# Kernel optimization log

Hardware: AMD Instinct MI355X
Metric: run time of the kernel (lower is better)

The kernel has to match this reference:

```python
import jax, jax.numpy as jnp
import numpy as np

B, H, S, D = 4, 16, 1024, 64


def setup_inputs() -> dict:
    key = jax.random.key(0)
    kq, kk, kv, kw = jax.random.split(key, 4)
    xq = jax.random.normal(kq, (B, H, S, D), dtype=jnp.float32)
    xk = jax.random.normal(kk, (B, H, S, D), dtype=jnp.float32)
    xv = jax.random.normal(kv, (B, H, S, D), dtype=jnp.float32)
    # wpsm: nn.Linear(n_heads, n_heads, bias=False) weight, shape [H_out, H_in]
    bound = 1.0 / np.sqrt(H)
    W = jax.random.uniform(kw, (H, H), minval=-bound, maxval=bound, dtype=jnp.float32)
    return {"xq": xq, "xk": xk, "xv": xv, "W": W, "causal": 1}


def reference(xq, xk, xv, W, causal):
    head_dim = xq.shape[-1]
    sq, sk = xq.shape[-2], xk.shape[-2]
    # QK^T scaled: [B, H, Sq, Sk]
    scores = jnp.einsum("bhqd,bhkd->bhqk", xq, xk) * jax.lax.rsqrt(jnp.float32(head_dim))
    # head-mixing linear over head axis: mixed[b,g,q,k] = sum_h W[g,h] * scores[b,h,q,k]
    scores = jnp.einsum("gh,bhqk->bgqk", W, scores)
    if causal:
        mask = jnp.triu(jnp.full((sq, sk), -jnp.inf, dtype=scores.dtype), k=1)
        scores = scores + mask  # broadcast over [B, H]
    probs = jax.nn.softmax(scores.astype(jnp.float32), axis=-1).astype(xq.dtype)
    out = jnp.einsum("bhqk,bhkd->bhqd", probs, xv)
    return out.transpose(0, 2, 1, 3)  # [B, Sq, H, D]
```

## Files before the change

### kernel.cpp

```cpp
#include <hip/hip_runtime.h>
#include <math.h>

#define NB 4
#define HH 16
#define SS 1024
#define DD 64
#define NKST 16

typedef __attribute__((ext_vector_type(8))) short bf16x8;
typedef __attribute__((ext_vector_type(4))) float f32x4;

static __device__ __forceinline__ short f2bf(float f) {
    __bf16 h = (__bf16)f;
    return __builtin_bit_cast(short, h);
}
static __device__ __forceinline__ float bflo(int w) {
    return __builtin_bit_cast(float, (unsigned)w << 16);
}
static __device__ __forceinline__ float bfhi(int w) {
    return __builtin_bit_cast(float, (unsigned)w & 0xffff0000u);
}
static __device__ __forceinline__ float bfu(unsigned short u) {
    return __builtin_bit_cast(float, (unsigned)u << 16);
}
static __device__ __forceinline__ int pidx(int pos, int hp) {
    int s = ((pos >> 2) & 3) | (((pos >> 9) & 1) << 2);
    return pos * 8 + (hp ^ s);
}
static __device__ __forceinline__ int midx(int g, int loc, int x3) {
    return g * 512 + ((((loc >> 2) ^ x3) << 2) | (loc & 3));
}

static __device__ __forceinline__ bf16x8 load8_bf16(const float* p) {
    const float4* p4 = reinterpret_cast<const float4*>(p);
    float4 a = p4[0], b = p4[1];
    bf16x8 f;
    f[0]=f2bf(a.x); f[1]=f2bf(a.y); f[2]=f2bf(a.z); f[3]=f2bf(a.w);
    f[4]=f2bf(b.x); f[5]=f2bf(b.y); f[6]=f2bf(b.z); f[7]=f2bf(b.w);
    return f;
}

__global__ __launch_bounds__(256) void prep_all(const float* __restrict__ xk,
                                                short* __restrict__ kfr,
                                                const float* __restrict__ xv,
                                                short* __restrict__ vfr) {
    __shared__ float T[64][65];
    const int bid = blockIdx.x;
    const int t = threadIdx.x;
    if (bid < 2048) {
        int c = bid * 256 + t;
        int lane = c & 63, ds = (c >> 6) & 1, kt = (c >> 7) & 3;
        int kst = (c >> 9) & 15, h = (c >> 13) & 15, b = c >> 17;
        const float* src = xk + ((size_t)((b * HH + h) * SS) + kst * 64 + kt * 16 + (lane & 15)) * DD
                              + ds * 32 + (lane >> 4) * 8;
        *(reinterpret_cast<bf16x8*>(kfr) + c) = load8_bf16(src);
    } else {
        int tile = bid - 2048;
        const float* src = xv + ((size_t)(tile >> 4) * SS + (tile & 15) * 64) * DD;
        int row = t >> 2, col = (t & 3) * 16;
#pragma unroll
        for (int ii = 0; ii < 4; ++ii) {
            float4 v = *reinterpret_cast<const float4*>(src + row * DD + col + ii * 4);
            T[row][col + ii*4] = v.x; T[row][col + ii*4 + 1] = v.y;
            T[row][col + ii*4 + 2] = v.z; T[row][col + ii*4 + 3] = v.w;
        }
        __syncthreads();
#pragma unroll
        for (int jj = 0; jj < 2; ++jj) {
            int c2 = t * 2 + jj;
            int lane = c2 & 63, nt = (c2 >> 6) & 3, kc = (c2 >> 8) & 1;
            bf16x8 o;
#pragma unroll
            for (int i = 0; i < 8; ++i)
                o[i] = f2bf(T[kc * 32 + (lane >> 4) * 8 + i][nt * 16 + (lane & 15)]);
            *(reinterpret_cast<bf16x8*>(vfr) + (size_t)tile * 512 + c2) = o;
        }
    }
}

__global__ __launch_bounds__(1024) void hca_fused(
    const float* __restrict__ xq, const short* __restrict__ kfr,
    const short* __restrict__ vfr, const float* __restrict__ Wm,
    const int* __restrict__ causalp, unsigned short* __restrict__ ppO,
    float2* __restrict__ ppml)
{
    __shared__ int Pbuf[8192];
    __shared__ int Mbuf[8192];

    const int tid  = threadIdx.x;
    const int lane = tid & 63;
    const int w    = tid >> 6;
    const int l15  = lane & 15;
    const int lg   = lane >> 4;

    const int bid  = blockIdx.x;
    const int b    = bid & 3;
    const int u    = (bid >> 2) & 63;
    const int r    = (bid >> 8) & 1;
    const int qt   = r ? u : 63 - u;
    const int kpar = u & 1;
    const int q0   = qt << 4;
    const int pairIdx = b * 64 + qt;

    const int causal = causalp[0];
    const int hp = w & 7;
    const int kh = w >> 3;
    const int g  = w;

    const float LOG2E = 1.44269504088896f;

    bf16x8 wt = {0,0,0,0,0,0,0,0};
    if (lg < 2) {
#pragma unroll
        for (int ii = 0; ii < 8; ++ii)
            wt[ii] = f2bf(Wm[l15 * 16 + lg * 8 + ii] * 0.125f * LOG2E);
    }

    const short* vb0 = vfr + (size_t)(b * HH + g) * NKST * 8 * 512 + lane * 8;
    const short* kb0 = kfr + (size_t)(b * HH + 2 * hp) * NKST * 8 * 512 + lane * 8;

    bf16x8 qf[2][2];
#pragma unroll
    for (int hi = 0; hi < 2; ++hi) {
        const float* qp = xq + ((size_t)(b * HH + 2 * hp + hi) * SS + q0 + l15) * DD + lg * 8;
#pragma unroll
        for (int ds = 0; ds < 2; ++ds) qf[hi][ds] = load8_bf16(qp + ds * 32);
    }

    f32x4 oacc[4];
#pragma unroll
    for (int nt = 0; nt < 4; ++nt) oacc[nt] = (f32x4){0.f, 0.f, 0.f, 0.f};
    float mrun = -INFINITY, lrun = 0.f;

    const int nkf = causal ? ((q0 + 16 + 63) >> 6) : NKST;

#pragma unroll 1
    for (int kst = kpar; kst < nkf; kst += 2) {
        const int k0 = kst << 6;

        const short* kbase = kb0 + (size_t)kst * 8 * 512;
        __builtin_amdgcn_s_setprio(1);
#pragma unroll
        for (int kt2 = 0; kt2 < 2; ++kt2) {
            const int kt = kh * 2 + kt2;
            f32x4 a0 = (f32x4){0.f,0.f,0.f,0.f}, a1 = a0;
#pragma unroll
            for (int ds = 0; ds < 2; ++ds) {
                bf16x8 kfa = *reinterpret_cast<const bf16x8*>(kbase + (kt*2 + ds) * 512);
                bf16x8 kfb = *reinterpret_cast<const bf16x8*>(kbase + (NKST*8 + kt*2 + ds) * 512);
                a0 = __builtin_amdgcn_mfma_f32_16x16x32_bf16(qf[0][ds], kfa, a0, 0, 0, 0);
                a1 = __builtin_amdgcn_mfma_f32_16x16x32_bf16(qf[1][ds], kfb, a1, 0, 0, 0);
            }
#pragma unroll
            for (int rr = 0; rr < 4; ++rr) {
                int pos = (lg * 4 + rr) * 64 + kt * 16 + l15;
                int pk = (int)(unsigned short)f2bf(a0[rr]) | ((int)(unsigned short)f2bf(a1[rr]) << 16);
                Pbuf[pidx(pos, hp)] = pk;
            }
        }
        __builtin_amdgcn_s_setprio(0);

        const short* vbase = vb0 + (size_t)kst * 8 * 512;
        bf16x8 vf[8];
#pragma unroll
        for (int kc = 0; kc < 2; ++kc)
#pragma unroll
            for (int nt = 0; nt < 4; ++nt)
                vf[kc * 4 + nt] = *reinterpret_cast<const bf16x8*>(vbase + (kc*4 + nt) * 512);

        __syncthreads();

#pragma unroll
        for (int m = 0; m < 4; ++m) {
            const int c = w * 4 + m;
            const int pos = c * 16 + l15;
            int4 ia = {0, 0, 0, 0};
            if (lg < 2) {
                ia.x = Pbuf[pidx(pos, lg * 4 + 0)];
                ia.y = Pbuf[pidx(pos, lg * 4 + 1)];
                ia.z = Pbuf[pidx(pos, lg * 4 + 2)];
                ia.w = Pbuf[pidx(pos, lg * 4 + 3)];
            }
            bf16x8 A = __builtin_bit_cast(bf16x8, ia);
            f32x4 cc = (f32x4){0.f, 0.f, 0.f, 0.f};
            cc = __builtin_amdgcn_mfma_f32_16x16x32_bf16(A, wt, cc, 0, 0, 0);
            int loc = w * 32 + (c & 3) * 8 + lg * 2;
            int x3 = (w + l15) & 7;
            int u0 = (int)(unsigned short)f2bf(cc[0]) | ((int)(unsigned short)f2bf(cc[1]) << 16);
            int u1 = (int)(unsigned short)f2bf(cc[2]) | ((int)(unsigned short)f2bf(cc[3]) << 16);
            *reinterpret_cast<int2*>(&Mbuf[midx(l15, loc, x3)]) = make_int2(u0, u1);
        }
        __syncthreads();

        const int x3r = (l15 + g) & 7;
        int4 rA = *reinterpret_cast<const int4*>(&Mbuf[midx(g, l15 * 32 + lg * 4, x3r)]);
        int4 rB = *reinterpret_cast<const int4*>(&Mbuf[midx(g, l15 * 32 + 16 + lg * 4, x3r)]);

        float sm[16];
#pragma unroll
        for (int jj = 0; jj < 4; ++jj) {
            sm[2*jj]     = bflo(rA[jj]);  sm[2*jj + 1] = bfhi(rA[jj]);
            sm[8 + 2*jj] = bflo(rB[jj]);  sm[9 + 2*jj] = bfhi(rB[jj]);
        }
        if (causal && kst == nkf - 1) {
#pragma unroll
            for (int jj = 0; jj < 16; ++jj) {
                int kk = (jj < 8) ? (lg * 8 + jj) : (32 + lg * 8 + (jj - 8));
                if (k0 + kk > q0 + l15) sm[jj] = -INFINITY;
            }
        }

        float mx[4];
#pragma unroll
        for (int t = 0; t < 4; ++t)
            mx[t] = fmaxf(fmaxf(sm[4*t], sm[4*t+1]), fmaxf(sm[4*t+2], sm[4*t+3]));
        float mt = fmaxf(fmaxf(mx[0], mx[1]), fmaxf(mx[2], mx[3]));
        mt = fmaxf(mt, __shfl_xor(mt, 16));
        mt = fmaxf(mt, __shfl_xor(mt, 32));

        if (__any(mt > mrun + 8.0f)) {
            float mnew = fmaxf(mrun, mt);
            float scl = __builtin_amdgcn_exp2f(mrun - mnew);
            mrun = mnew;
            lrun *= scl;
            int scli = __builtin_bit_cast(int, scl);
#pragma unroll
            for (int rr = 0; rr < 4; ++rr) {
                int v = __builtin_amdgcn_ds_bpermute((lg * 4 + rr) * 4, scli);
                float s = __builtin_bit_cast(float, v);
#pragma unroll
                for (int nt = 0; nt < 4; ++nt) oacc[nt][rr] *= s;
            }
        }

#pragma unroll
        for (int jj = 0; jj < 16; ++jj) sm[jj] = __builtin_amdgcn_exp2f(sm[jj] - mrun);
        float s0 = ((sm[0]+sm[1]) + (sm[2]+sm[3])) + ((sm[4]+sm[5]) + (sm[6]+sm[7]));
        float s1 = ((sm[8]+sm[9]) + (sm[10]+sm[11])) + ((sm[12]+sm[13]) + (sm[14]+sm[15]));
        lrun += s0 + s1;

        int paw[8];
#pragma unroll
        for (int t = 0; t < 8; ++t)
            paw[t] = (int)(unsigned short)f2bf(sm[2*t]) | ((int)(unsigned short)f2bf(sm[2*t+1]) << 16);
        bf16x8 pa0 = __builtin_bit_cast(bf16x8, *(int4*)&paw[0]);
        bf16x8 pa1 = __builtin_bit_cast(bf16x8, *(int4*)&paw[4]);

        __builtin_amdgcn_s_setprio(1);
#pragma unroll
        for (int nt = 0; nt < 4; ++nt)
            oacc[nt] = __builtin_amdgcn_mfma_f32_16x16x32_bf16(pa0, vf[nt], oacc[nt], 0, 0, 0);
#pragma unroll
        for (int nt = 0; nt < 4; ++nt)
            oacc[nt] = __builtin_amdgcn_mfma_f32_16x16x32_bf16(pa1, vf[4 + nt], oacc[nt], 0, 0, 0);
        __builtin_amdgcn_s_setprio(0);
    }

    float lt = lrun;
    lt += __shfl_xor(lt, 16);
    lt += __shfl_xor(lt, 32);
    if (lg == 0)
        ppml[(((size_t)pairIdx * 2 + kpar) * 16 + g) * 16 + l15] = make_float2(mrun, lt);
    float rl = (lt > 0.f) ? (1.0f / lt) : 0.f;
    int rli = __builtin_bit_cast(int, rl);
    size_t obase = (((size_t)pairIdx * 2 + kpar) * 16 + g) * 1024;
#pragma unroll
    for (int rr = 0; rr < 4; ++rr) {
        int v = __builtin_amdgcn_ds_bpermute((lg * 4 + rr) * 4, rli);
        float linv = __builtin_bit_cast(float, v);
        int q = lg * 4 + rr;
#pragma unroll
        for (int nt = 0; nt < 4; ++nt)
            ppO[obase + q * 64 + nt * 16 + l15] =
                (unsigned short)f2bf(oacc[nt][rr] * linv);
    }
}

__global__ __launch_bounds__(256) void hca_combine(
    const unsigned short* __restrict__ ppO, const float2* __restrict__ ppml,
    float* __restrict__ out)
{
    const int pairIdx = blockIdx.x;
    const int b = pairIdx >> 6, qt = pairIdx & 63;
    const int t = threadIdx.x;
    const int g = t >> 4, dc = t & 15;

    const size_t o0 = (((size_t)pairIdx * 2 + 0) * 16 + g) * 1024;
    const size_t o1 = (((size_t)pairIdx * 2 + 1) * 16 + g) * 1024;
    const float2* ml0p = ppml + (((size_t)pairIdx * 2 + 0) * 16 + g) * 16;
    const float2* ml1p = ppml + (((size_t)pairIdx * 2 + 1) * 16 + g) * 16;

#pragma unroll 4
    for (int q = 0; q < 16; ++q) {
        float2 ml0 = ml0p[q], ml1 = ml1p[q];
        float ms = fmaxf(ml0.x, ml1.x);
        float w0 = ml0.y * exp2f(ml0.x - ms);
        float w1 = ml1.y * exp2f(ml1.x - ms);
        float rs = 1.0f / (w0 + w1);
        float a0 = w0 * rs, a1 = w1 * rs;
        ushort4 u0 = *reinterpret_cast<const ushort4*>(ppO + o0 + q * 64 + dc * 4);
        ushort4 u1 = *reinterpret_cast<const ushort4*>(ppO + o1 + q * 64 + dc * 4);
        float4 res;
        res.x = a0 * bfu(u0.x) + a1 * bfu(u1.x);
        res.y = a0 * bfu(u0.y) + a1 * bfu(u1.y);
        res.z = a0 * bfu(u0.z) + a1 * bfu(u1.z);
        res.w = a0 * bfu(u0.w) + a1 * bfu(u1.w);
        *reinterpret_cast<float4*>(out + (((size_t)b * SS + qt * 16 + q) * HH + g) * DD + dc * 4) = res;
    }
}

extern "C" void kernel_launch(void* const* d_in, const int* in_sizes, int n_in,
                              void* d_out, int out_size, void* d_ws, size_t ws_size,
                              hipStream_t stream) {
    const float* xq = (const float*)d_in[0];
    const float* xk = (const float*)d_in[1];
    const float* xv = (const float*)d_in[2];
    const float* Wm = (const float*)d_in[3];
    const int* causal = (const int*)d_in[4];
    float* out = (float*)d_out;

    short* vfr = (short*)d_ws;
    short* kfr = vfr + (size_t)NB * HH * SS * DD;
    unsigned short* ppO = (unsigned short*)(kfr + (size_t)NB * HH * SS * DD);
    float2* ppml = (float2*)(ppO + (size_t)512 * 16 * 1024);

    prep_all<<<2048 + NB * HH * NKST, 256, 0, stream>>>(xk, kfr, xv, vfr);

    hca_fused<<<512, 1024, 0, stream>>>(xq, kfr, vfr, Wm, causal, ppO, ppml);
    hca_combine<<<256, 256, 0, stream>>>(ppO, ppml, out);
}
```

Before: 80.13 us.

## Software-pipeline head-mix and softmax stages across K tiles with double-buffered LDS

```diff
diff --git a/kernel.cpp b/kernel.cpp
--- a/kernel.cpp
+++ b/kernel.cpp
@@ -47,24 +47,29 @@
     __shared__ float T[64][65];
     const int bid = blockIdx.x;
     const int t = threadIdx.x;
-    if (bid < 2048) {
-        int c = bid * 256 + t;
-        int lane = c & 63, ds = (c >> 6) & 1, kt = (c >> 7) & 3;
-        int kst = (c >> 9) & 15, h = (c >> 13) & 15, b = c >> 17;
-        const float* src = xk + ((size_t)((b * HH + h) * SS) + kst * 64 + kt * 16 + (lane & 15)) * DD
-                              + ds * 32 + (lane >> 4) * 8;
-        *(reinterpret_cast<bf16x8*>(kfr) + c) = load8_bf16(src);
+    const bool isK = bid < 1024;
+    const int tile = isK ? bid : bid - 1024;
+    const float* src = (isK ? xk : xv) + ((size_t)(tile >> 4) * SS + (tile & 15) * 64) * DD;
+    int row = t >> 2, col = (t & 3) * 16;
+#pragma unroll
+    for (int ii = 0; ii < 4; ++ii) {
+        float4 v = *reinterpret_cast<const float4*>(src + row * DD + col + ii * 4);
+        T[row][col + ii*4] = v.x; T[row][col + ii*4 + 1] = v.y;
+        T[row][col + ii*4 + 2] = v.z; T[row][col + ii*4 + 3] = v.w;
+    }
+    __syncthreads();
+    if (isK) {
+#pragma unroll
+        for (int jj = 0; jj < 2; ++jj) {
+            int c2 = t * 2 + jj;
+            int lane = c2 & 63, ds = (c2 >> 6) & 1, kt = (c2 >> 7) & 3;
+            bf16x8 o;
+#pragma unroll
+            for (int i = 0; i < 8; ++i)
+                o[i] = f2bf(T[kt * 16 + (lane & 15)][ds * 32 + (lane >> 4) * 8 + i]);
+            *(reinterpret_cast<bf16x8*>(kfr) + (size_t)tile * 512 + c2) = o;
+        }
     } else {
-        int tile = bid - 2048;
-        const float* src = xv + ((size_t)(tile >> 4) * SS + (tile & 15) * 64) * DD;
-        int row = t >> 2, col = (t & 3) * 16;
-#pragma unroll
-        for (int ii = 0; ii < 4; ++ii) {
-            float4 v = *reinterpret_cast<const float4*>(src + row * DD + col + ii * 4);
-            T[row][col + ii*4] = v.x; T[row][col + ii*4 + 1] = v.y;
-            T[row][col + ii*4 + 2] = v.z; T[row][col + ii*4 + 3] = v.w;
-        }
-        __syncthreads();
 #pragma unroll
         for (int jj = 0; jj < 2; ++jj) {
             int c2 = t * 2 + jj;
@@ -85,7 +90,7 @@
     float2* __restrict__ ppml)
 {
     __shared__ int Pbuf[8192];
-    __shared__ int Mbuf[8192];
+    __shared__ int Mbuf[2][8192];
 
     const int tid  = threadIdx.x;
     const int lane = tid & 63;
@@ -103,9 +108,8 @@
     const int pairIdx = b * 64 + qt;
 
     const int causal = causalp[0];
-    const int hp = w & 7;
-    const int kh = w >> 3;
-    const int g  = w;
+    const int h = w;
+    const int g = w;
 
     const float LOG2E = 1.44269504088896f;
 
@@ -116,15 +120,14 @@
             wt[ii] = f2bf(Wm[l15 * 16 + lg * 8 + ii] * 0.125f * LOG2E);
     }
 
-    const short* vb0 = vfr + (size_t)(b * HH + g) * NKST * 8 * 512 + lane * 8;
-    const short* kb0 = kfr + (size_t)(b * HH + 2 * hp) * NKST * 8 * 512 + lane * 8;
-
-    bf16x8 qf[2][2];
-#pragma unroll
-    for (int hi = 0; hi < 2; ++hi) {
-        const float* qp = xq + ((size_t)(b * HH + 2 * hp + hi) * SS + q0 + l15) * DD + lg * 8;
-#pragma unroll
-        for (int ds = 0; ds < 2; ++ds) qf[hi][ds] = load8_bf16(qp + ds * 32);
+    const short* kb0 = kfr + (size_t)(b * HH + h) * NKST * 4096 + lane * 8;
+    const short* vb0 = vfr + (size_t)(b * HH + g) * NKST * 4096 + lane * 8;
+
+    bf16x8 qf[2];
+    {
+        const float* qp = xq + ((size_t)(b * HH + h) * SS + q0 + l15) * DD + lg * 8;
+        qf[0] = load8_bf16(qp);
+        qf[1] = load8_bf16(qp + 32);
     }
 
     f32x4 oacc[4];
@@ -133,43 +136,112 @@
     float mrun = -INFINITY, lrun = 0.f;
 
     const int nkf = causal ? ((q0 + 16 + 63) >> 6) : NKST;
-
-#pragma unroll 1
-    for (int kst = kpar; kst < nkf; kst += 2) {
-        const int k0 = kst << 6;
-
-        const short* kbase = kb0 + (size_t)kst * 8 * 512;
-        __builtin_amdgcn_s_setprio(1);
-#pragma unroll
-        for (int kt2 = 0; kt2 < 2; ++kt2) {
-            const int kt = kh * 2 + kt2;
-            f32x4 a0 = (f32x4){0.f,0.f,0.f,0.f}, a1 = a0;
+    const int n   = (nkf > kpar) ? ((nkf - kpar + 1) >> 1) : 0;
+
+    auto runA = [&](int kst) {
+        const short* kbase = kb0 + (size_t)kst * 4096;
+#pragma unroll
+        for (int kt = 0; kt < 4; ++kt) {
+            f32x4 a = (f32x4){0.f, 0.f, 0.f, 0.f};
 #pragma unroll
             for (int ds = 0; ds < 2; ++ds) {
-                bf16x8 kfa = *reinterpret_cast<const bf16x8*>(kbase + (kt*2 + ds) * 512);
-                bf16x8 kfb = *reinterpret_cast<const bf16x8*>(kbase + (NKST*8 + kt*2 + ds) * 512);
-                a0 = __builtin_amdgcn_mfma_f32_16x16x32_bf16(qf[0][ds], kfa, a0, 0, 0, 0);
-                a1 = __builtin_amdgcn_mfma_f32_16x16x32_bf16(qf[1][ds], kfb, a1, 0, 0, 0);
+                bf16x8 kf = *reinterpret_cast<const bf16x8*>(kbase + (kt*2 + ds) * 512);
+                a = __builtin_amdgcn_mfma_f32_16x16x32_bf16(qf[ds], kf, a, 0, 0, 0);
             }
 #pragma unroll
             for (int rr = 0; rr < 4; ++rr) {
                 int pos = (lg * 4 + rr) * 64 + kt * 16 + l15;
-                int pk = (int)(unsigned short)f2bf(a0[rr]) | ((int)(unsigned short)f2bf(a1[rr]) << 16);
-                Pbuf[pidx(pos, hp)] = pk;
-            }
-        }
-        __builtin_amdgcn_s_setprio(0);
-
-        const short* vbase = vb0 + (size_t)kst * 8 * 512;
-        bf16x8 vf[8];
-#pragma unroll
-        for (int kc = 0; kc < 2; ++kc)
-#pragma unroll
-            for (int nt = 0; nt < 4; ++nt)
-                vf[kc * 4 + nt] = *reinterpret_cast<const bf16x8*>(vbase + (kc*4 + nt) * 512);
-
+                reinterpret_cast<short*>(Pbuf)[pidx(pos, h >> 1) * 2 + (h & 1)] = f2bf(a[rr]);
+            }
+        }
+    };
+
+    bf16x8 vA = {0,0,0,0,0,0,0,0}, vB = vA;
+
+    auto runD = [&](int sd, const int* Mb) {
+        const short* vbase = vb0 + (size_t)sd * 4096;
+        bf16x8 v01 = *reinterpret_cast<const bf16x8*>(vbase + 1 * 512);
+        bf16x8 v11 = *reinterpret_cast<const bf16x8*>(vbase + 5 * 512);
+
+        const int x3r = (l15 + g) & 7;
+        int4 rA = *reinterpret_cast<const int4*>(&Mb[midx(g, l15 * 32 + lg * 4, x3r)]);
+        int4 rB = *reinterpret_cast<const int4*>(&Mb[midx(g, l15 * 32 + 16 + lg * 4, x3r)]);
+
+        float sm[16];
+#pragma unroll
+        for (int jj = 0; jj < 4; ++jj) {
+            sm[2*jj]     = bflo(rA[jj]);  sm[2*jj + 1] = bfhi(rA[jj]);
+            sm[8 + 2*jj] = bflo(rB[jj]);  sm[9 + 2*jj] = bfhi(rB[jj]);
+        }
+        if (causal && sd == nkf - 1) {
+            const int k0 = sd << 6;
+#pragma unroll
+            for (int jj = 0; jj < 16; ++jj) {
+                int kk = (jj < 8) ? (lg * 8 + jj) : (32 + lg * 8 + (jj - 8));
+                if (k0 + kk > q0 + l15) sm[jj] = -INFINITY;
+            }
+        }
+
+        float mx[4];
+#pragma unroll
+        for (int t = 0; t < 4; ++t)
+            mx[t] = fmaxf(fmaxf(sm[4*t], sm[4*t+1]), fmaxf(sm[4*t+2], sm[4*t+3]));
+        float mt = fmaxf(fmaxf(mx[0], mx[1]), fmaxf(mx[2], mx[3]));
+        mt = fmaxf(mt, __shfl_xor(mt, 16));
+        mt = fmaxf(mt, __shfl_xor(mt, 32));
+
+        if (__any(mt > mrun + 8.0f)) {
+            float mnew = fmaxf(mrun, mt);
+            float scl = __builtin_amdgcn_exp2f(mrun - mnew);
+            mrun = mnew;
+            lrun *= scl;
+            int scli = __builtin_bit_cast(int, scl);
+#pragma unroll
+            for (int rr = 0; rr < 4; ++rr) {
+                int v = __builtin_amdgcn_ds_bpermute((lg * 4 + rr) * 4, scli);
+                float s = __builtin_bit_cast(float, v);
+#pragma unroll
+                for (int nt = 0; nt < 4; ++nt) oacc[nt][rr] *= s;
+            }
+        }
+
+        bf16x8 v02 = *reinterpret_cast<const bf16x8*>(vbase + 2 * 512);
+        bf16x8 v12 = *reinterpret_cast<const bf16x8*>(vbase + 6 * 512);
+
+#pragma unroll
+        for (int jj = 0; jj < 16; ++jj) sm[jj] = __builtin_amdgcn_exp2f(sm[jj] - mrun);
+        float s0 = ((sm[0]+sm[1]) + (sm[2]+sm[3])) + ((sm[4]+sm[5]) + (sm[6]+sm[7]));
+        float s1 = ((sm[8]+sm[9]) + (sm[10]+sm[11])) + ((sm[12]+sm[13]) + (sm[14]+sm[15]));
+        lrun += s0 + s1;
+
+        bf16x8 v03 = *reinterpret_cast<const bf16x8*>(vbase + 3 * 512);
+        bf16x8 v13 = *reinterpret_cast<const bf16x8*>(vbase + 7 * 512);
+
+        int paw[8];
+#pragma unroll
+        for (int t = 0; t < 8; ++t)
+            paw[t] = (int)(unsigned short)f2bf(sm[2*t]) | ((int)(unsigned short)f2bf(sm[2*t+1]) << 16);
+        bf16x8 pa0 = __builtin_bit_cast(bf16x8, *(int4*)&paw[0]);
+        bf16x8 pa1 = __builtin_bit_cast(bf16x8, *(int4*)&paw[4]);
+
+        oacc[0] = __builtin_amdgcn_mfma_f32_16x16x32_bf16(pa0, vA,  oacc[0], 0, 0, 0);
+        oacc[0] = __builtin_amdgcn_mfma_f32_16x16x32_bf16(pa1, vB,  oacc[0], 0, 0, 0);
+        oacc[1] = __builtin_amdgcn_mfma_f32_16x16x32_bf16(pa0, v01, oacc[1], 0, 0, 0);
+        oacc[1] = __builtin_amdgcn_mfma_f32_16x16x32_bf16(pa1, v11, oacc[1], 0, 0, 0);
+        oacc[2] = __builtin_amdgcn_mfma_f32_16x16x32_bf16(pa0, v02, oacc[2], 0, 0, 0);
+        oacc[2] = __builtin_amdgcn_mfma_f32_16x16x32_bf16(pa1, v12, oacc[2], 0, 0, 0);
+        oacc[3] = __builtin_amdgcn_mfma_f32_16x16x32_bf16(pa0, v03, oacc[3], 0, 0, 0);
+        oacc[3] = __builtin_amdgcn_mfma_f32_16x16x32_bf16(pa1, v13, oacc[3], 0, 0, 0);
+    };
+
+    if (n > 0) runA(kpar);
+
+#pragma unroll 1
+    for (int i = 0; i < n; ++i) {
+        const int si = kpar + 2 * i;
         __syncthreads();
 
+        int* Mb = &Mbuf[i & 1][0];
 #pragma unroll
         for (int m = 0; m < 4; ++m) {
             const int c = w * 4 + m;
@@ -188,73 +260,22 @@
             int x3 = (w + l15) & 7;
             int u0 = (int)(unsigned short)f2bf(cc[0]) | ((int)(unsigned short)f2bf(cc[1]) << 16);
             int u1 = (int)(unsigned short)f2bf(cc[2]) | ((int)(unsigned short)f2bf(cc[3]) << 16);
-            *reinterpret_cast<int2*>(&Mbuf[midx(l15, loc, x3)]) = make_int2(u0, u1);
-        }
+            *reinterpret_cast<int2*>(&Mb[midx(l15, loc, x3)]) = make_int2(u0, u1);
+        }
+
+        if (i > 0) runD(si - 2, &Mbuf[(i - 1) & 1][0]);
+
         __syncthreads();
 
-        const int x3r = (l15 + g) & 7;
-        int4 rA = *reinterpret_cast<const int4*>(&Mbuf[midx(g, l15 * 32 + lg * 4, x3r)]);
-        int4 rB = *reinterpret_cast<const int4*>(&Mbuf[midx(g, l15 * 32 + 16 + lg * 4, x3r)]);
-
-        float sm[16];
-#pragma unroll
-        for (int jj = 0; jj < 4; ++jj) {
-            sm[2*jj]     = bflo(rA[jj]);  sm[2*jj + 1] = bfhi(rA[jj]);
-            sm[8 + 2*jj] = bflo(rB[jj]);  sm[9 + 2*jj] = bfhi(rB[jj]);
-        }
-        if (causal && kst == nkf - 1) {
-#pragma unroll
-            for (int jj = 0; jj < 16; ++jj) {
-                int kk = (jj < 8) ? (lg * 8 + jj) : (32 + lg * 8 + (jj - 8));
-                if (k0 + kk > q0 + l15) sm[jj] = -INFINITY;
-            }
-        }
-
-        float mx[4];
-#pragma unroll
-        for (int t = 0; t < 4; ++t)
-            mx[t] = fmaxf(fmaxf(sm[4*t], sm[4*t+1]), fmaxf(sm[4*t+2], sm[4*t+3]));
-        float mt = fmaxf(fmaxf(mx[0], mx[1]), fmaxf(mx[2], mx[3]));
-        mt = fmaxf(mt, __shfl_xor(mt, 16));
-        mt = fmaxf(mt, __shfl_xor(mt, 32));
-
-        if (__any(mt > mrun + 8.0f)) {
-            float mnew = fmaxf(mrun, mt);
-            float scl = __builtin_amdgcn_exp2f(mrun - mnew);
-            mrun = mnew;
-            lrun *= scl;
-            int scli = __builtin_bit_cast(int, scl);
-#pragma unroll
-            for (int rr = 0; rr < 4; ++rr) {
-                int v = __builtin_amdgcn_ds_bpermute((lg * 4 + rr) * 4, scli);
-                float s = __builtin_bit_cast(float, v);
-#pragma unroll
-                for (int nt = 0; nt < 4; ++nt) oacc[nt][rr] *= s;
-            }
-        }
-
-#pragma unroll
-        for (int jj = 0; jj < 16; ++jj) sm[jj] = __builtin_amdgcn_exp2f(sm[jj] - mrun);
-        float s0 = ((sm[0]+sm[1]) + (sm[2]+sm[3])) + ((sm[4]+sm[5]) + (sm[6]+sm[7]));
-        float s1 = ((sm[8]+sm[9]) + (sm[10]+sm[11])) + ((sm[12]+sm[13]) + (sm[14]+sm[15]));
-        lrun += s0 + s1;
-
-        int paw[8];
-#pragma unroll
-        for (int t = 0; t < 8; ++t)
-            paw[t] = (int)(unsigned short)f2bf(sm[2*t]) | ((int)(unsigned short)f2bf(sm[2*t+1]) << 16);
-        bf16x8 pa0 = __builtin_bit_cast(bf16x8, *(int4*)&paw[0]);
-        bf16x8 pa1 = __builtin_bit_cast(bf16x8, *(int4*)&paw[4]);
-
-        __builtin_amdgcn_s_setprio(1);
-#pragma unroll
-        for (int nt = 0; nt < 4; ++nt)
-            oacc[nt] = __builtin_amdgcn_mfma_f32_16x16x32_bf16(pa0, vf[nt], oacc[nt], 0, 0, 0);
-#pragma unroll
-        for (int nt = 0; nt < 4; ++nt)
-            oacc[nt] = __builtin_amdgcn_mfma_f32_16x16x32_bf16(pa1, vf[4 + nt], oacc[nt], 0, 0, 0);
-        __builtin_amdgcn_s_setprio(0);
-    }
+        if (i + 1 < n) runA(si + 2);
+
+        {
+            const short* vbase = vb0 + (size_t)si * 4096;
+            vA = *reinterpret_cast<const bf16x8*>(vbase + 0 * 512);
+            vB = *reinterpret_cast<const bf16x8*>(vbase + 4 * 512);
+        }
+    }
+    if (n > 0) runD(kpar + 2 * (n - 1), &Mbuf[(n - 1) & 1][0]);
 
     float lt = lrun;
     lt += __shfl_xor(lt, 16);
@@ -324,7 +345,7 @@
     unsigned short* ppO = (unsigned short*)(kfr + (size_t)NB * HH * SS * DD);
     float2* ppml = (float2*)(ppO + (size_t)512 * 16 * 1024);
 
-    prep_all<<<2048 + NB * HH * NKST, 256, 0, stream>>>(xk, kfr, xv, vfr);
+    prep_all<<<2048, 256, 0, stream>>>(xk, kfr, xv, vfr);
 
     hca_fused<<<512, 1024, 0, stream>>>(xq, kfr, vfr, Wm, causal, ppO, ppml);
     hca_combine<<<256, 256, 0, stream>>>(ppO, ppml, out);
```

Result: no change. 80.54 us (+0.5%).

## Stage K prep through LDS tiles and use lighter LDS-only barriers in fused kernel

Applied to the files above, without the earlier changes.

```diff
diff --git a/kernel.cpp b/kernel.cpp
--- a/kernel.cpp
+++ b/kernel.cpp
@@ -22,6 +22,9 @@
 }
 static __device__ __forceinline__ float bfu(unsigned short u) {
     return __builtin_bit_cast(float, (unsigned)u << 16);
+}
+static __device__ __forceinline__ void lds_barrier() {
+    asm volatile("s_waitcnt lgkmcnt(0)\n\ts_barrier" ::: "memory");
 }
 static __device__ __forceinline__ int pidx(int pos, int hp) {
     int s = ((pos >> 2) & 3) | (((pos >> 9) & 1) << 2);
@@ -47,24 +50,29 @@
     __shared__ float T[64][65];
     const int bid = blockIdx.x;
     const int t = threadIdx.x;
-    if (bid < 2048) {
-        int c = bid * 256 + t;
-        int lane = c & 63, ds = (c >> 6) & 1, kt = (c >> 7) & 3;
-        int kst = (c >> 9) & 15, h = (c >> 13) & 15, b = c >> 17;
-        const float* src = xk + ((size_t)((b * HH + h) * SS) + kst * 64 + kt * 16 + (lane & 15)) * DD
-                              + ds * 32 + (lane >> 4) * 8;
-        *(reinterpret_cast<bf16x8*>(kfr) + c) = load8_bf16(src);
+    const bool isK = bid < 1024;
+    const int tile = isK ? bid : bid - 1024;
+    const float* src = (isK ? xk : xv) + ((size_t)(tile >> 4) * SS + (tile & 15) * 64) * DD;
+    int row = t >> 2, col = (t & 3) * 16;
+#pragma unroll
+    for (int ii = 0; ii < 4; ++ii) {
+        float4 v = *reinterpret_cast<const float4*>(src + row * DD + col + ii * 4);
+        T[row][col + ii*4] = v.x; T[row][col + ii*4 + 1] = v.y;
+        T[row][col + ii*4 + 2] = v.z; T[row][col + ii*4 + 3] = v.w;
+    }
+    __syncthreads();
+    if (isK) {
+#pragma unroll
+        for (int jj = 0; jj < 2; ++jj) {
+            int c2 = t * 2 + jj;
+            int lane = c2 & 63, ds = (c2 >> 6) & 1, kt = (c2 >> 7) & 3;
+            bf16x8 o;
+#pragma unroll
+            for (int i = 0; i < 8; ++i)
+                o[i] = f2bf(T[kt * 16 + (lane & 15)][ds * 32 + (lane >> 4) * 8 + i]);
+            *(reinterpret_cast<bf16x8*>(kfr) + (size_t)tile * 512 + c2) = o;
+        }
     } else {
-        int tile = bid - 2048;
-        const float* src = xv + ((size_t)(tile >> 4) * SS + (tile & 15) * 64) * DD;
-        int row = t >> 2, col = (t & 3) * 16;
-#pragma unroll
-        for (int ii = 0; ii < 4; ++ii) {
-            float4 v = *reinterpret_cast<const float4*>(src + row * DD + col + ii * 4);
-            T[row][col + ii*4] = v.x; T[row][col + ii*4 + 1] = v.y;
-            T[row][col + ii*4 + 2] = v.z; T[row][col + ii*4 + 3] = v.w;
-        }
-        __syncthreads();
 #pragma unroll
         for (int jj = 0; jj < 2; ++jj) {
             int c2 = t * 2 + jj;
@@ -168,7 +176,7 @@
             for (int nt = 0; nt < 4; ++nt)
                 vf[kc * 4 + nt] = *reinterpret_cast<const bf16x8*>(vbase + (kc*4 + nt) * 512);
 
-        __syncthreads();
+        lds_barrier();
 
 #pragma unroll
         for (int m = 0; m < 4; ++m) {
@@ -190,7 +198,7 @@
             int u1 = (int)(unsigned short)f2bf(cc[2]) | ((int)(unsigned short)f2bf(cc[3]) << 16);
             *reinterpret_cast<int2*>(&Mbuf[midx(l15, loc, x3)]) = make_int2(u0, u1);
         }
-        __syncthreads();
+        lds_barrier();
 
         const int x3r = (l15 + g) & 7;
         int4 rA = *reinterpret_cast<const int4*>(&Mbuf[midx(g, l15 * 32 + lg * 4, x3r)]);
@@ -324,7 +332,7 @@
     unsigned short* ppO = (unsigned short*)(kfr + (size_t)NB * HH * SS * DD);
     float2* ppml = (float2*)(ppO + (size_t)512 * 16 * 1024);
 
-    prep_all<<<2048 + NB * HH * NKST, 256, 0, stream>>>(xk, kfr, xv, vfr);
+    prep_all<<<2048, 256, 0, stream>>>(xk, kfr, xv, vfr);
 
     hca_fused<<<512, 1024, 0, stream>>>(xq, kfr, vfr, Wm, causal, ppO, ppml);
     hca_combine<<<256, 256, 0, stream>>>(ppO, ppml, out);
```

New measurement: 80.11 us. Within noise of the previous version (-0.0%).
